# Optimization experiments

Measured on AMD Instinct MI355X. Metric: run time of the kernel, lower is better.

Reference implementation:

```python
import jax, jax.numpy as jnp
import numpy as np

N_RAYS, N_SAMPLES, HIDDEN, N_VOXELS = 8192, 256, 64, 1000


def setup_inputs() -> dict:
    key = jax.random.key(0)
    ks = jax.random.split(key, 10)
    ray_start = jax.random.normal(ks[0], (N_RAYS, 3), jnp.float32)
    ray_dir = jax.random.normal(ks[1], (N_RAYS, 3), jnp.float32)
    ray_dir = ray_dir / jnp.linalg.norm(ray_dir, axis=-1, keepdims=True)
    # monotonically increasing depths along each ray
    sampled_depth = jnp.sort(jax.random.uniform(ks[2], (N_RAYS, N_SAMPLES), jnp.float32) * 4.0 + 0.5, axis=-1)
    sampled_dists = jax.random.uniform(ks[3], (N_RAYS, N_SAMPLES), jnp.float32) * 0.02 + 1e-3
    sampled_idx = jax.random.randint(ks[4], (N_RAYS, N_SAMPLES), -333, N_VOXELS).astype(jnp.int64)
    W1 = jax.random.normal(ks[5], (3, HIDDEN), jnp.float32) * 0.5
    b1 = jnp.zeros((HIDDEN,), jnp.float32)
    w_sigma = jax.random.normal(ks[6], (HIDDEN,), jnp.float32) * 0.5
    W_rgb = jax.random.normal(ks[7], (HIDDEN, 3), jnp.float32) * 0.5
    W_dir = jax.random.normal(ks[8], (3, 3), jnp.float32) * 0.5
    b_rgb = jnp.zeros((3,), jnp.float32)
    return {"ray_start": ray_start, "ray_dir": ray_dir, "sampled_depth": sampled_depth,
            "sampled_dists": sampled_dists, "sampled_idx": sampled_idx,
            "W1": W1, "b1": b1, "w_sigma": w_sigma, "W_rgb": W_rgb, "W_dir": W_dir, "b_rgb": b_rgb}


def _volume_render(ray_start, ray_dir, sampled_depth, sampled_dists, sampled_idx,
                   W1, b1, w_sigma, W_rgb, W_dir, b_rgb):
    # sampled_xyz = ray(ray_start, ray_dir, depth)
    xyz = ray_start[:, None, :] + ray_dir[:, None, :] * sampled_depth[..., None]  # [N,P,3]
    h = jax.nn.relu(jnp.einsum('npi,ih->nph', xyz, W1) + b1)                      # [N,P,H]
    sigma = jnp.einsum('nph,h->np', h, w_sigma)                                   # [N,P]
    rgb = jax.nn.sigmoid(jnp.einsum('nph,hc->npc', h, W_rgb)
                         + jnp.einsum('ni,ic->nc', ray_dir, W_dir)[:, None, :] + b_rgb)  # [N,P,3]
    mask = (sampled_idx != -1).astype(sigma.dtype)                                # [N,P]
    # free_energy = relu(sigma) * dists * 7.0, scattered back with zeros at misses
    free_energy = jax.nn.relu(sigma) * sampled_dists * 7.0 * mask
    shifted = jnp.concatenate([jnp.zeros_like(free_energy[:, :1]), free_energy[:, :-1]], axis=-1)
    a = 1.0 - jnp.exp(-free_energy)
    b = jnp.exp(-jnp.cumsum(shifted, axis=-1))
    probs = a * b                                                                 # [N,P]
    depths = jnp.sum(sampled_depth * probs, axis=-1)                              # [N]
    missed = 1.0 - jnp.sum(probs, axis=-1)                                        # [N]
    colors = jnp.sum(rgb * probs[..., None], axis=-2)                             # [N,3]
    return jnp.concatenate([colors, depths[:, None], missed[:, None], probs], axis=-1)  # [N, 3+1+1+P]


def reference(ray_start, ray_dir, sampled_depth, sampled_dists, sampled_idx,
              W1, b1, w_sigma, W_rgb, W_dir, b_rgb):
    return _volume_render(ray_start, ray_dir, sampled_depth, sampled_dists, sampled_idx,
                          W1, b1, w_sigma, W_rgb, W_dir, b_rgb)
```

## Files before the change

### kernel.cpp

```cpp
#include <hip/hip_runtime.h>

#define NRAYS 8192
#define NS    256
#define HID   64
#define NPAIR 32
#define NP4   16
#define RPB   4
#define SPT   4

typedef _Float16 f16x2 __attribute__((ext_vector_type(2)));

static __device__ __forceinline__ float fdot2(f16x2 a, f16x2 b, float c) {
    return __builtin_amdgcn_fdot2(a, b, c, false);
}
static __device__ __forceinline__ f16x2 mk2(float a, float b) {
    f16x2 v; v.x = (_Float16)a; v.y = (_Float16)b; return v;
}

struct __align__(16) W4  { f16x2 ws, wr, wg, wb; };
struct __align__(16) AB4 { f16x2 A01, B01, A23, B23; };

__global__ __launch_bounds__(256, 8) void vr_kernel(
    const float* __restrict__ ray_start,
    const float* __restrict__ ray_dir,
    const float* __restrict__ sampled_depth,
    const float* __restrict__ sampled_dists,
    const int*   __restrict__ sampled_idx,
    const float* __restrict__ W1,
    const float* __restrict__ b1,
    const float* __restrict__ w_sigma,
    const float* __restrict__ W_rgb,
    const float* __restrict__ W_dir,
    const float* __restrict__ b_rgb,
    float* __restrict__ out)
{
    __shared__ W4  sW[NPAIR];
    __shared__ AB4 sAB[RPB][NP4];

    const int t = threadIdx.x;
    if (t < NPAIR) {
        const int h0 = 2*t, h1 = 2*t + 1;
        W4 w;
        w.ws = mk2(w_sigma[h0],    w_sigma[h1]);
        w.wr = mk2(W_rgb[h0*3+0],  W_rgb[h1*3+0]);
        w.wg = mk2(W_rgb[h0*3+1],  W_rgb[h1*3+1]);
        w.wb = mk2(W_rgb[h0*3+2],  W_rgb[h1*3+2]);
        sW[t] = w;
    }
    {
        const int rr  = t >> 6;
        const int h   = t & 63;
        const int ray = blockIdx.x * RPB + rr;
        const float ox = ray_start[ray*3+0], oy = ray_start[ray*3+1], oz = ray_start[ray*3+2];
        const float dx = ray_dir[ray*3+0],  dy = ray_dir[ray*3+1],  dz = ray_dir[ray*3+2];
        const float w0 = W1[h], w1 = W1[HID + h], w2 = W1[2*HID + h];
        const float A = fmaf(w0, ox, fmaf(w1, oy, fmaf(w2, oz, b1[h])));
        const float B = fmaf(w0, dx, fmaf(w1, dy, w2 * dz));
        const int i = h >> 2, m = h & 3;
        _Float16* dst16 = (_Float16*)&sAB[rr][i];
        dst16[(m >> 1) * 4 + (m & 1)]     = (_Float16)A;
        dst16[(m >> 1) * 4 + (m & 1) + 2] = (_Float16)B;
    }
    __syncthreads();

    const int lane = t & 63;
    const int wv   = t >> 6;
    const int ray  = blockIdx.x * RPB + wv;

    const float dx = ray_dir[ray*3+0], dy = ray_dir[ray*3+1], dz = ray_dir[ray*3+2];
    const float dwr = fmaf(dx, W_dir[0], fmaf(dy, W_dir[3], fmaf(dz, W_dir[6], b_rgb[0])));
    const float dwg = fmaf(dx, W_dir[1], fmaf(dy, W_dir[4], fmaf(dz, W_dir[7], b_rgb[1])));
    const float dwb = fmaf(dx, W_dir[2], fmaf(dy, W_dir[5], fmaf(dz, W_dir[8], b_rgb[2])));

    const size_t rbase = (size_t)ray * NS + (size_t)lane * SPT;
    const float4 dep = *(const float4*)(sampled_depth + rbase);
    const float4 dst = *(const float4*)(sampled_dists + rbase);
    const int4  vidx = *(const int4*)(sampled_idx + rbase);

    const float dpt[SPT] = {dep.x, dep.y, dep.z, dep.w};
    const float dsv[SPT] = {dst.x, dst.y, dst.z, dst.w};
    const int   vid[SPT] = {vidx.x, vidx.y, vidx.z, vidx.w};

    f16x2 d2[SPT];
#pragma unroll
    for (int j = 0; j < SPT; ++j) d2[j] = mk2(dpt[j], dpt[j]);
    const f16x2 zero2 = mk2(0.f, 0.f);

    float sig[SPT] = {0,0,0,0};
    float cr[SPT]  = {0,0,0,0};
    float cg[SPT]  = {0,0,0,0};
    float cb[SPT]  = {0,0,0,0};

#pragma unroll 2
    for (int i = 0; i < NP4; ++i) {
        const W4  w0 = sW[2*i];
        const W4  w1 = sW[2*i + 1];
        const AB4 ab = sAB[wv][i];
#pragma unroll
        for (int j = 0; j < SPT; ++j) {
            f16x2 hv0 = __builtin_elementwise_fma(ab.B01, d2[j], ab.A01);
            f16x2 hv1 = __builtin_elementwise_fma(ab.B23, d2[j], ab.A23);
            hv0 = __builtin_elementwise_max(hv0, zero2);
            hv1 = __builtin_elementwise_max(hv1, zero2);
            sig[j] = fdot2(hv0, w0.ws, sig[j]);
            cr[j]  = fdot2(hv0, w0.wr, cr[j]);
            cg[j]  = fdot2(hv0, w0.wg, cg[j]);
            cb[j]  = fdot2(hv0, w0.wb, cb[j]);
            sig[j] = fdot2(hv1, w1.ws, sig[j]);
            cr[j]  = fdot2(hv1, w1.wr, cr[j]);
            cg[j]  = fdot2(hv1, w1.wg, cg[j]);
            cb[j]  = fdot2(hv1, w1.wb, cb[j]);
        }
    }

    float c[SPT];
    float run = 0.f;
#pragma unroll
    for (int j = 0; j < SPT; ++j) {
        float f = fmaxf(sig[j], 0.f) * dsv[j] * 7.0f;
        if (vid[j] == -1) f = 0.f;
        run += f;
        c[j] = run;
    }

    float tot = run;
#pragma unroll
    for (int off = 1; off < 64; off <<= 1) {
        const float v = __shfl_up(tot, off, 64);
        if (lane >= off) tot += v;
    }
    const float base = tot - run;

    float Eprev = __expf(-base);
    float prob[SPT];
    float s0 = 0.f, s1 = 0.f, s2 = 0.f, s3 = 0.f, s4 = 0.f;
#pragma unroll
    for (int j = 0; j < SPT; ++j) {
        const float Ej = __expf(-(base + c[j]));
        const float p  = Eprev - Ej;
        Eprev = Ej;
        prob[j] = p;
        const float rr = __builtin_amdgcn_rcpf(1.f + __expf(-(cr[j] + dwr)));
        const float gg = __builtin_amdgcn_rcpf(1.f + __expf(-(cg[j] + dwg)));
        const float bb = __builtin_amdgcn_rcpf(1.f + __expf(-(cb[j] + dwb)));
        s0 += p;
        s1 = fmaf(dpt[j], p, s1);
        s2 = fmaf(rr, p, s2);
        s3 = fmaf(gg, p, s3);
        s4 = fmaf(bb, p, s4);
    }

#pragma unroll
    for (int off = 32; off >= 1; off >>= 1) {
        s0 += __shfl_xor(s0, off, 64);
        s1 += __shfl_xor(s1, off, 64);
        s2 += __shfl_xor(s2, off, 64);
        s3 += __shfl_xor(s3, off, 64);
        s4 += __shfl_xor(s4, off, 64);
    }

    float* orow = out + (size_t)ray * (NS + 5);
#pragma unroll
    for (int j = 0; j < SPT; ++j)
        orow[5 + SPT*lane + j] = prob[j];

    if (lane == 0) {
        orow[0] = s2;
        orow[1] = s3;
        orow[2] = s4;
        orow[3] = s1;
        orow[4] = 1.f - s0;
    }
}

extern "C" void kernel_launch(void* const* d_in, const int* in_sizes, int n_in,
                              void* d_out, int out_size, void* d_ws, size_t ws_size,
                              hipStream_t stream)
{
    vr_kernel<<<NRAYS / RPB, 256, 0, stream>>>(
        (const float*)d_in[0],
        (const float*)d_in[1],
        (const float*)d_in[2],
        (const float*)d_in[3],
        (const int*)  d_in[4],
        (const float*)d_in[5],
        (const float*)d_in[6],
        (const float*)d_in[7],
        (const float*)d_in[8],
        (const float*)d_in[9],
        (const float*)d_in[10],
        (float*)d_out);
}
```

Baseline: 108.2 us.

## Compute hidden-layer projections with MFMA 16x16x32 f16 instead of fdot2 loops

Replaces the per-thread packed-f16 dot-product loop over hidden units with matrix-core MFMA instructions. Each wave builds relu hidden activations for 16 samples at a time in f16x8 fragments and multiplies them against a 64x4 weight fragment (sigma and rgb, padded to 16 columns). Results are staged through shared memory and transposed back to a per-lane layout for the scan and compositing. This wastes most MFMA output columns and adds LDS round trips and block syncs, and the prob stores are also moved ahead of the shuffle reduction.

New measurement: 106.0 us. -2.0%, faster.

```diff
diff --git a/kernel.cpp b/kernel.cpp
--- a/kernel.cpp
+++ b/kernel.cpp
@@ -3,24 +3,14 @@
 #define NRAYS 8192
 #define NS    256
 #define HID   64
-#define NPAIR 32
-#define NP4   16
 #define RPB   4
-#define SPT   4
+#define EP    264
 
 typedef _Float16 f16x2 __attribute__((ext_vector_type(2)));
+typedef _Float16 f16x8 __attribute__((ext_vector_type(8)));
+typedef float    f32x4 __attribute__((ext_vector_type(4)));
 
-static __device__ __forceinline__ float fdot2(f16x2 a, f16x2 b, float c) {
-    return __builtin_amdgcn_fdot2(a, b, c, false);
-}
-static __device__ __forceinline__ f16x2 mk2(float a, float b) {
-    f16x2 v; v.x = (_Float16)a; v.y = (_Float16)b; return v;
-}
-
-struct __align__(16) W4  { f16x2 ws, wr, wg, wb; };
-struct __align__(16) AB4 { f16x2 A01, B01, A23, B23; };
-
-__global__ __launch_bounds__(256, 8) void vr_kernel(
+__global__ __launch_bounds__(256) void vr_kernel(
     const float* __restrict__ ray_start,
     const float* __restrict__ ray_dir,
     const float* __restrict__ sampled_depth,
@@ -34,90 +24,97 @@
     const float* __restrict__ b_rgb,
     float* __restrict__ out)
 {
-    __shared__ W4  sW[NPAIR];
-    __shared__ AB4 sAB[RPB][NP4];
+    __shared__ _Float16 sA[RPB][HID];
+    __shared__ _Float16 sB[RPB][HID];
+    __shared__ _Float16 sDep[RPB][NS];
+    __shared__ float    sE[RPB][4][EP];
 
-    const int t = threadIdx.x;
-    if (t < NPAIR) {
-        const int h0 = 2*t, h1 = 2*t + 1;
-        W4 w;
-        w.ws = mk2(w_sigma[h0],    w_sigma[h1]);
-        w.wr = mk2(W_rgb[h0*3+0],  W_rgb[h1*3+0]);
-        w.wg = mk2(W_rgb[h0*3+1],  W_rgb[h1*3+1]);
-        w.wb = mk2(W_rgb[h0*3+2],  W_rgb[h1*3+2]);
-        sW[t] = w;
-    }
-    {
-        const int rr  = t >> 6;
-        const int h   = t & 63;
-        const int ray = blockIdx.x * RPB + rr;
-        const float ox = ray_start[ray*3+0], oy = ray_start[ray*3+1], oz = ray_start[ray*3+2];
-        const float dx = ray_dir[ray*3+0],  dy = ray_dir[ray*3+1],  dz = ray_dir[ray*3+2];
-        const float w0 = W1[h], w1 = W1[HID + h], w2 = W1[2*HID + h];
-        const float A = fmaf(w0, ox, fmaf(w1, oy, fmaf(w2, oz, b1[h])));
-        const float B = fmaf(w0, dx, fmaf(w1, dy, w2 * dz));
-        const int i = h >> 2, m = h & 3;
-        _Float16* dst16 = (_Float16*)&sAB[rr][i];
-        dst16[(m >> 1) * 4 + (m & 1)]     = (_Float16)A;
-        dst16[(m >> 1) * 4 + (m & 1) + 2] = (_Float16)B;
-    }
-    __syncthreads();
-
+    const int t    = threadIdx.x;
     const int lane = t & 63;
     const int wv   = t >> 6;
     const int ray  = blockIdx.x * RPB + wv;
 
-    const float dx = ray_dir[ray*3+0], dy = ray_dir[ray*3+1], dz = ray_dir[ray*3+2];
+    const float ox = ray_start[ray*3+0], oy = ray_start[ray*3+1], oz = ray_start[ray*3+2];
+    const float dx = ray_dir[ray*3+0],  dy = ray_dir[ray*3+1],  dz = ray_dir[ray*3+2];
+    {
+        const int h = lane;
+        const float w0 = W1[h], w1 = W1[HID + h], w2 = W1[2*HID + h];
+        const float A = fmaf(w0, ox, fmaf(w1, oy, fmaf(w2, oz, b1[h])));
+        const float B = fmaf(w0, dx, fmaf(w1, dy, w2 * dz));
+        sA[wv][h] = (_Float16)A;
+        sB[wv][h] = (_Float16)B;
+    }
+
     const float dwr = fmaf(dx, W_dir[0], fmaf(dy, W_dir[3], fmaf(dz, W_dir[6], b_rgb[0])));
     const float dwg = fmaf(dx, W_dir[1], fmaf(dy, W_dir[4], fmaf(dz, W_dir[7], b_rgb[1])));
     const float dwb = fmaf(dx, W_dir[2], fmaf(dy, W_dir[5], fmaf(dz, W_dir[8], b_rgb[2])));
 
-    const size_t rbase = (size_t)ray * NS + (size_t)lane * SPT;
+    const size_t rbase = (size_t)ray * NS + (size_t)lane * 4;
     const float4 dep = *(const float4*)(sampled_depth + rbase);
     const float4 dst = *(const float4*)(sampled_dists + rbase);
     const int4  vidx = *(const int4*)(sampled_idx + rbase);
 
-    const float dpt[SPT] = {dep.x, dep.y, dep.z, dep.w};
-    const float dsv[SPT] = {dst.x, dst.y, dst.z, dst.w};
-    const int   vid[SPT] = {vidx.x, vidx.y, vidx.z, vidx.w};
+    {
+        f16x2 dl; dl.x = (_Float16)dep.x; dl.y = (_Float16)dep.y;
+        f16x2 dh; dh.x = (_Float16)dep.z; dh.y = (_Float16)dep.w;
+        f16x2* dp = (f16x2*)&sDep[wv][4*lane];
+        dp[0] = dl; dp[1] = dh;
+    }
 
-    f16x2 d2[SPT];
+    const int n = lane & 15;
+    const int q = lane >> 4;
+    f16x8 bflo = (f16x8)(_Float16)0.f;
+    f16x8 bfhi = (f16x8)(_Float16)0.f;
+    if (n < 4) {
 #pragma unroll
-    for (int j = 0; j < SPT; ++j) d2[j] = mk2(dpt[j], dpt[j]);
-    const f16x2 zero2 = mk2(0.f, 0.f);
-
-    float sig[SPT] = {0,0,0,0};
-    float cr[SPT]  = {0,0,0,0};
-    float cg[SPT]  = {0,0,0,0};
-    float cb[SPT]  = {0,0,0,0};
-
-#pragma unroll 2
-    for (int i = 0; i < NP4; ++i) {
-        const W4  w0 = sW[2*i];
-        const W4  w1 = sW[2*i + 1];
-        const AB4 ab = sAB[wv][i];
-#pragma unroll
-        for (int j = 0; j < SPT; ++j) {
-            f16x2 hv0 = __builtin_elementwise_fma(ab.B01, d2[j], ab.A01);
-            f16x2 hv1 = __builtin_elementwise_fma(ab.B23, d2[j], ab.A23);
-            hv0 = __builtin_elementwise_max(hv0, zero2);
-            hv1 = __builtin_elementwise_max(hv1, zero2);
-            sig[j] = fdot2(hv0, w0.ws, sig[j]);
-            cr[j]  = fdot2(hv0, w0.wr, cr[j]);
-            cg[j]  = fdot2(hv0, w0.wg, cg[j]);
-            cb[j]  = fdot2(hv0, w0.wb, cb[j]);
-            sig[j] = fdot2(hv1, w1.ws, sig[j]);
-            cr[j]  = fdot2(hv1, w1.wr, cr[j]);
-            cg[j]  = fdot2(hv1, w1.wg, cg[j]);
-            cb[j]  = fdot2(hv1, w1.wb, cb[j]);
+        for (int j = 0; j < 8; ++j) {
+            const int klo = q*8 + j, khi = 32 + q*8 + j;
+            const float vlo = (n == 0) ? w_sigma[klo] : W_rgb[klo*3 + (n-1)];
+            const float vhi = (n == 0) ? w_sigma[khi] : W_rgb[khi*3 + (n-1)];
+            bflo[j] = (_Float16)vlo;
+            bfhi[j] = (_Float16)vhi;
         }
     }
+    __syncthreads();
 
-    float c[SPT];
+    const f16x8 Alo = *(const f16x8*)&sA[wv][q*8];
+    const f16x8 Ahi = *(const f16x8*)&sA[wv][32 + q*8];
+    const f16x8 Blo = *(const f16x8*)&sB[wv][q*8];
+    const f16x8 Bhi = *(const f16x8*)&sB[wv][32 + q*8];
+    const f16x8 z8  = (f16x8)(_Float16)0.f;
+
+#pragma unroll
+    for (int tt = 0; tt < 16; ++tt) {
+        const _Float16 dv = sDep[wv][16*tt + n];
+        f16x8 d8;
+#pragma unroll
+        for (int j = 0; j < 8; ++j) d8[j] = dv;
+        f16x8 hlo = __builtin_elementwise_fma(Blo, d8, Alo);
+        f16x8 hhi = __builtin_elementwise_fma(Bhi, d8, Ahi);
+        hlo = __builtin_elementwise_max(hlo, z8);
+        hhi = __builtin_elementwise_max(hhi, z8);
+        f32x4 acc = {0.f, 0.f, 0.f, 0.f};
+        acc = __builtin_amdgcn_mfma_f32_16x16x32_f16(hlo, bflo, acc, 0, 0, 0);
+        acc = __builtin_amdgcn_mfma_f32_16x16x32_f16(hhi, bfhi, acc, 0, 0, 0);
+        if (n < 4)
+            *(f32x4*)&sE[wv][n][16*tt + 4*q] = acc;
+    }
+    __syncthreads();
+
+    const f32x4 sg4 = *(const f32x4*)&sE[wv][0][4*lane];
+    const f32x4 cr4 = *(const f32x4*)&sE[wv][1][4*lane];
+    const f32x4 cg4 = *(const f32x4*)&sE[wv][2][4*lane];
+    const f32x4 cb4 = *(const f32x4*)&sE[wv][3][4*lane];
+
+    const float dpt[4] = {dep.x, dep.y, dep.z, dep.w};
+    const float dsv[4] = {dst.x, dst.y, dst.z, dst.w};
+    const int   vid[4] = {vidx.x, vidx.y, vidx.z, vidx.w};
+
+    float c[4];
     float run = 0.f;
 #pragma unroll
-    for (int j = 0; j < SPT; ++j) {
-        float f = fmaxf(sig[j], 0.f) * dsv[j] * 7.0f;
+    for (int j = 0; j < 4; ++j) {
+        float f = fmaxf(sg4[j], 0.f) * dsv[j] * 7.0f;
         if (vid[j] == -1) f = 0.f;
         run += f;
         c[j] = run;
@@ -132,23 +129,28 @@
     const float base = tot - run;
 
     float Eprev = __expf(-base);
-    float prob[SPT];
+    float prob[4];
     float s0 = 0.f, s1 = 0.f, s2 = 0.f, s3 = 0.f, s4 = 0.f;
 #pragma unroll
-    for (int j = 0; j < SPT; ++j) {
+    for (int j = 0; j < 4; ++j) {
         const float Ej = __expf(-(base + c[j]));
         const float p  = Eprev - Ej;
         Eprev = Ej;
         prob[j] = p;
-        const float rr = __builtin_amdgcn_rcpf(1.f + __expf(-(cr[j] + dwr)));
-        const float gg = __builtin_amdgcn_rcpf(1.f + __expf(-(cg[j] + dwg)));
-        const float bb = __builtin_amdgcn_rcpf(1.f + __expf(-(cb[j] + dwb)));
+        const float rr = __builtin_amdgcn_rcpf(1.f + __expf(-(cr4[j] + dwr)));
+        const float gg = __builtin_amdgcn_rcpf(1.f + __expf(-(cg4[j] + dwg)));
+        const float bb = __builtin_amdgcn_rcpf(1.f + __expf(-(cb4[j] + dwb)));
         s0 += p;
         s1 = fmaf(dpt[j], p, s1);
         s2 = fmaf(rr, p, s2);
         s3 = fmaf(gg, p, s3);
         s4 = fmaf(bb, p, s4);
     }
+
+    float* orow = out + (size_t)ray * (NS + 5);
+#pragma unroll
+    for (int j = 0; j < 4; ++j)
+        orow[5 + 4*lane + j] = prob[j];
 
 #pragma unroll
     for (int off = 32; off >= 1; off >>= 1) {
@@ -158,11 +160,6 @@
         s3 += __shfl_xor(s3, off, 64);
         s4 += __shfl_xor(s4, off, 64);
     }
-
-    float* orow = out + (size_t)ray * (NS + 5);
-#pragma unroll
-    for (int j = 0; j < SPT; ++j)
-        orow[5 + SPT*lane + j] = prob[j];
 
     if (lane == 0) {
         orow[0] = s2;
```
